# Performance work log

Hardware: AMD Instinct MI355X
Metric: run time of the kernel (lower is better)

Reference implementation:

```python
import jax, jax.numpy as jnp
import numpy as np

B, S, OBS, H, A, L = 512, 512, 64, 128, 9, 2
LN_EPS = 1e-5


def setup_inputs() -> dict:
    key = jax.random.key(0)
    ks = jax.random.split(key, 32)
    sc = 0.05
    inp = {
        'obs': jax.random.normal(ks[0], (B, S, OBS), jnp.float32),
        'masks': (jax.random.uniform(ks[1], (B, S)) > 0.01).astype(jnp.float32),
        'noise': jax.random.normal(ks[2], (B, S, A), jnp.float32),
        # encoder: Linear(OBS,H) -> LayerNorm(H) -> ReLU -> Linear(H,H) -> ReLU
        'enc_w1': jax.random.normal(ks[3], (H, OBS)) * sc,
        'enc_b1': jnp.zeros((H,)),
        'ln_g': jnp.ones((H,)),
        'ln_b': jnp.zeros((H,)),
        'enc_w2': jax.random.normal(ks[4], (H, H)) * sc,
        'enc_b2': jnp.zeros((H,)),
        # 2-layer LSTM, torch gate order [i, f, g, o]
        'wih0': jax.random.normal(ks[5], (4 * H, H)) * sc,
        'whh0': jax.random.normal(ks[6], (4 * H, H)) * sc,
        'bih0': jnp.zeros((4 * H,)),
        'bhh0': jnp.zeros((4 * H,)),
        'wih1': jax.random.normal(ks[7], (4 * H, H)) * sc,
        'whh1': jax.random.normal(ks[8], (4 * H, H)) * sc,
        'bih1': jnp.zeros((4 * H,)),
        'bhh1': jnp.zeros((4 * H,)),
        # actor mean head: Linear(H,H//2) -> ReLU -> Linear(H//2,A) -> Tanh
        'am_w1': jax.random.normal(ks[9], (H // 2, H)) * sc,
        'am_b1': jnp.zeros((H // 2,)),
        'am_w2': jax.random.normal(ks[10], (A, H // 2)) * sc,
        'am_b2': jnp.zeros((A,)),
        'log_std': jnp.full((A,), -1.0, jnp.float32),
        # critic head: Linear(H,H//2) -> ReLU -> Linear(H//2,1)
        'cr_w1': jax.random.normal(ks[11], (H // 2, H)) * sc,
        'cr_b1': jnp.zeros((H // 2,)),
        'cr_w2': jax.random.normal(ks[12], (1, H // 2)) * sc,
        'cr_b2': jnp.zeros((1,)),
    }
    return inp


def _encoder(x, w1, b1, g, b, w2, b2):
    y = x @ w1.T + b1
    mu = y.mean(-1, keepdims=True)
    var = y.var(-1, keepdims=True)
    y = (y - mu) * jax.lax.rsqrt(var + LN_EPS) * g + b
    y = jax.nn.relu(y)
    return jax.nn.relu(y @ w2.T + b2)


def _masked_lstm(enc, masks, wih, whh, bih, bhh):
    # enc: (B,S,H), masks: (B,S). Carry h,c: (L,B,H). Reset h,c by mask, then step.
    h0 = jnp.zeros((L, enc.shape[0], H), enc.dtype)
    c0 = jnp.zeros_like(h0)

    def step(carry, xs):
        h, c = carry
        x_t, m_t = xs  # (B,H), (B,1)
        h = h * m_t
        c = c * m_t
        hs, cs = [], []
        inp = x_t
        for l in range(L):
            gates = inp @ wih[l].T + bih[l] + h[l] @ whh[l].T + bhh[l]
            i, f, g, o = jnp.split(gates, 4, axis=-1)
            c_l = jax.nn.sigmoid(f) * c[l] + jax.nn.sigmoid(i) * jnp.tanh(g)
            h_l = jax.nn.sigmoid(o) * jnp.tanh(c_l)
            hs.append(h_l)
            cs.append(c_l)
            inp = h_l
        return (jnp.stack(hs), jnp.stack(cs)), inp

    xs = (enc.transpose(1, 0, 2), masks.T[:, :, None])  # time-major
    (h, c), outs = jax.lax.scan(step, (h0, c0), xs)
    return outs.transpose(1, 0, 2), h, c  # (B,S,H)


def reference(obs, masks, noise, enc_w1, enc_b1, ln_g, ln_b, enc_w2, enc_b2,
              wih0, whh0, bih0, bhh0, wih1, whh1, bih1, bhh1,
              am_w1, am_b1, am_w2, am_b2, log_std, cr_w1, cr_b1, cr_w2, cr_b2):
    enc = _encoder(obs, enc_w1, enc_b1, ln_g, ln_b, enc_w2, enc_b2)
    lstm_out, h, c = _masked_lstm(enc, masks, (wih0, wih1), (whh0, whh1),
                                  (bih0, bih1), (bhh0, bhh1))
    mean = jnp.tanh(jax.nn.relu(lstm_out @ am_w1.T + am_b1) @ am_w2.T + am_b2)
    ls = jnp.clip(log_std, -4.0, 0.0)
    std = jnp.exp(ls)
    action = jax.lax.stop_gradient(mean + std * noise)  # dist.sample()
    z = (action - mean) / std
    log_prob = (-0.5 * z * z - ls - 0.5 * jnp.log(2.0 * jnp.pi)).sum(-1)
    value = (jax.nn.relu(lstm_out @ cr_w1.T + cr_b1) @ cr_w2.T + cr_b2)[..., 0]
    return action, log_prob, value, h, c
```

## Files before the change

kernel.cpp:

```cpp
#include <hip/hip_runtime.h>
#include <hip/hip_bf16.h>
#include <math.h>


#define DEV __device__ __forceinline__

typedef __attribute__((ext_vector_type(4))) float f4;
typedef __attribute__((ext_vector_type(8))) short s16x8;

static constexpr int Bsz = 512, Ssz = 512, OBSD = 64, HD = 128, AD = 9;
static constexpr int TOK = Bsz * Ssz;

static constexpr size_t LP_OFF  = (size_t)TOK * AD;
static constexpr size_t VAL_OFF = LP_OFF + TOK;
static constexpr size_t H_OFF   = VAL_OFF + TOK;
static constexpr size_t C_OFF   = H_OFF + 2 * Bsz * HD;

static constexpr size_t WS_SEQ   = 0;
static constexpr size_t WS_WIH1B = (size_t)TOK * HD * 2;
static constexpr size_t WS_AMW1B = WS_WIH1B + 512 * 128 * 2;
static constexpr size_t WS_AMW2P = WS_AMW1B + 64 * 128 * 2;
static constexpr size_t WS_CRW1B = WS_AMW2P + 16 * 64 * 2;
static constexpr size_t WS_CRW2P = WS_CRW1B + 64 * 128 * 2;

static constexpr int L_H0  = 131072;
static constexpr int L_H1  = 139264;
static constexpr int L_MKB = 147456;
static constexpr int L_TOT = 149504;

DEV unsigned short f2bf(float f) {
  union { float f; unsigned u; } v; v.f = f;
  unsigned r = v.u + 0x7fffu + ((v.u >> 16) & 1u);
  return (unsigned short)(r >> 16);
}
DEV s16x8 cvt8(f4 a, f4 b) {
  s16x8 r;
  r[0]=(short)f2bf(a[0]); r[1]=(short)f2bf(a[1]); r[2]=(short)f2bf(a[2]); r[3]=(short)f2bf(a[3]);
  r[4]=(short)f2bf(b[0]); r[5]=(short)f2bf(b[1]); r[6]=(short)f2bf(b[2]); r[7]=(short)f2bf(b[3]);
  return r;
}
DEV f4 splat4(float v) { f4 r = {v, v, v, v}; return r; }
DEV f4 mfma16(s16x8 a, s16x8 b, f4 c) {
  return __builtin_amdgcn_mfma_f32_16x16x32_bf16(a, b, c, 0, 0, 0);
}
DEV float fexp2(float x) { return __builtin_amdgcn_exp2f(x); }
DEV float frcp(float x)  { return __builtin_amdgcn_rcpf(x); }
DEV float sigm(float x)   { return frcp(1.f + fexp2(-1.4426950408889634f * x)); }
DEV float tanh_f(float x) { return 2.f * frcp(1.f + fexp2(-2.8853900817779268f * x)) - 1.f; }

__global__ void k_prep(const float* __restrict__ wih1, const float* __restrict__ amw1,
                       const float* __restrict__ amw2, const float* __restrict__ crw1,
                       const float* __restrict__ crw2,
                       unsigned short* __restrict__ wih1b, unsigned short* __restrict__ amw1b,
                       unsigned short* __restrict__ amw2p, unsigned short* __restrict__ crw1b,
                       unsigned short* __restrict__ crw2p)
{
  int i = blockIdx.x * 256 + threadIdx.x;
  if (i < 65536) wih1b[i] = f2bf(wih1[i]);
  if (i < 8192) { amw1b[i] = f2bf(amw1[i]); crw1b[i] = f2bf(crw1[i]); }
  if (i < 1024) {
    int n = i >> 6, k = i & 63;
    amw2p[i] = (n < 9) ? f2bf(amw2[n * 64 + k]) : (unsigned short)0;
    crw2p[i] = (n == 0) ? f2bf(crw2[k]) : (unsigned short)0;
  }
}

__global__ __launch_bounds__(256) void k_encoder(
    const float* __restrict__ obs,
    const float* __restrict__ w1, const float* __restrict__ b1,
    const float* __restrict__ lng, const float* __restrict__ lnb,
    const float* __restrict__ w2, const float* __restrict__ b2,
    unsigned short* __restrict__ enc)
{
  __shared__ unsigned short sy[4][2048];
  const int tid = threadIdx.x, lane = tid & 63, wv = tid >> 6;
  const int cl = lane & 15, grp = lane >> 4;
  const size_t tok0 = ((size_t)blockIdx.x * 4 + wv) * 16;

  s16x8 aob[2];
  {
    const float* p = obs + (tok0 + cl) * 64 + grp * 8;
    aob[0] = cvt8(*(const f4*)p, *(const f4*)(p + 4));
    aob[1] = cvt8(*(const f4*)(p + 32), *(const f4*)(p + 36));
  }

  f4 acc[8];
#pragma unroll
  for (int n = 0; n < 8; ++n) acc[n] = splat4(0.f);
#pragma unroll
  for (int kk = 0; kk < 2; ++kk)
#pragma unroll
    for (int n = 0; n < 8; ++n) {
      const float* p = w1 + (size_t)(n * 16 + cl) * 64 + kk * 32 + grp * 8;
      acc[n] = mfma16(aob[kk], cvt8(*(const f4*)p, *(const f4*)(p + 4)), acc[n]);
    }

  float y[8][4], s[4] = {0,0,0,0}, q[4] = {0,0,0,0};
#pragma unroll
  for (int n = 0; n < 8; ++n) {
    float bb = b1[n * 16 + cl];
#pragma unroll
    for (int i = 0; i < 4; ++i) { float v = acc[n][i] + bb; y[n][i] = v; s[i] += v; q[i] += v * v; }
  }
#pragma unroll
  for (int i = 0; i < 4; ++i)
    for (int m = 1; m < 16; m <<= 1) { s[i] += __shfl_xor(s[i], m); q[i] += __shfl_xor(q[i], m); }
  float mean[4], rstd[4];
#pragma unroll
  for (int i = 0; i < 4; ++i) {
    mean[i] = s[i] * (1.f / 128.f);
    float var = q[i] * (1.f / 128.f) - mean[i] * mean[i];
    rstd[i] = rsqrtf(var + 1e-5f);
  }
  unsigned short* my = sy[wv];
#pragma unroll
  for (int n = 0; n < 8; ++n) {
    float gg = lng[n * 16 + cl], bb = lnb[n * 16 + cl];
#pragma unroll
    for (int i = 0; i < 4; ++i) {
      float v = (y[n][i] - mean[i]) * rstd[i] * gg + bb;
      v = v > 0.f ? v : 0.f;
      int row = grp * 4 + i;
      *(unsigned short*)((char*)my + row * 256 + (((n * 16 + cl) * 2) ^ ((row & 7) << 4))) = f2bf(v);
    }
  }
  __syncthreads();

  f4 acc2[8];
#pragma unroll
  for (int n = 0; n < 8; ++n) acc2[n] = splat4(0.f);
#pragma unroll
  for (int kk = 0; kk < 4; ++kk) {
    s16x8 a2 = *(const s16x8*)((char*)my + cl * 256 + ((kk * 64 + grp * 16) ^ ((cl & 7) << 4)));
#pragma unroll
    for (int n = 0; n < 8; ++n) {
      const float* p = w2 + (size_t)(n * 16 + cl) * 128 + kk * 32 + grp * 8;
      acc2[n] = mfma16(a2, cvt8(*(const f4*)p, *(const f4*)(p + 4)), acc2[n]);
    }
  }
#pragma unroll
  for (int n = 0; n < 8; ++n) {
    float bb = b2[n * 16 + cl];
#pragma unroll
    for (int i = 0; i < 4; ++i) {
      float v = acc2[n][i] + bb; v = v > 0.f ? v : 0.f;
      enc[(tok0 + grp * 4 + i) * 128 + n * 16 + cl] = f2bf(v);
    }
  }
}

__global__ __launch_bounds__(512, 2) void k_lstm(
    const unsigned short* enc_in,
    unsigned short* lstm_out,
    const float* __restrict__ masks,
    const float* __restrict__ wih0f, const float* __restrict__ whh0f,
    const float* __restrict__ bih0, const float* __restrict__ bhh0,
    const unsigned short* __restrict__ wih1b, const float* __restrict__ whh1f,
    const float* __restrict__ bih1, const float* __restrict__ bhh1,
    float* __restrict__ out_h, float* __restrict__ out_c)
{
  extern __shared__ char sm[];
  unsigned int* s_mkb = (unsigned int*)(sm + L_MKB);

  const int tid = threadIdx.x, lane = tid & 63, wv = tid >> 6;
  const int cl = lane & 15, grp = lane >> 4;
  const int b0 = blockIdx.x * 16, u0 = wv * 16;
  const s16x8 z8 = {0,0,0,0,0,0,0,0};

  for (int idx = tid; idx < 8192; idx += 512) {
    int row = idx >> 4, c8 = idx & 15;
    const float* p = wih0f + (size_t)row * 128 + c8 * 8;
    s16x8 v = cvt8(*(const f4*)p, *(const f4*)(p + 4));
    *(s16x8*)(sm + row * 256 + ((c8 * 16) ^ ((row & 7) << 4))) = v;
  }
  for (int idx = tid; idx < 4096; idx += 512)
    ((unsigned int*)(sm + L_H0))[idx] = 0;
  {
    int t = tid;
    unsigned int m = 0;
#pragma unroll
    for (int r = 0; r < 16; ++r)
      m |= (masks[(size_t)(b0 + r) * 512 + t] != 0.f ? 1u : 0u) << r;
    s_mkb[t] = m;
  }

  s16x8 Bh0[4][4], Bh1[4][4];
#pragma unroll
  for (int g = 0; g < 4; ++g)
#pragma unroll
    for (int kk = 0; kk < 4; ++kk) {
      const float* p0 = whh0f + (size_t)(g * 128 + u0 + cl) * 128 + kk * 32 + grp * 8;
      Bh0[g][kk] = cvt8(*(const f4*)p0, *(const f4*)(p0 + 4));
      const float* p1 = whh1f + (size_t)(g * 128 + u0 + cl) * 128 + kk * 32 + grp * 8;
      Bh1[g][kk] = cvt8(*(const f4*)p1, *(const f4*)(p1 + 4));
    }
  float bias0[4], bias1[4];
#pragma unroll
  for (int g = 0; g < 4; ++g) {
    bias0[g] = bih0[g * 128 + u0 + cl] + bhh0[g * 128 + u0 + cl];
    bias1[g] = bih1[g * 128 + u0 + cl] + bhh1[g * 128 + u0 + cl];
  }
  float c0[4] = {0,0,0,0}, c1[4] = {0,0,0,0};
  float h0r[4] = {0,0,0,0}, h1r[4] = {0,0,0,0};

  const int swz = (cl & 7) << 4;
  int hoff[4];
#pragma unroll
  for (int kk = 0; kk < 4; ++kk) hoff[kk] = cl * 256 + ((kk * 64 + grp * 16) ^ swz);
  const char* w0l = sm + (u0 + cl) * 256;
  const unsigned short* encl = enc_in + (size_t)(b0 + cl) * 65536 + grp * 8;
  const unsigned short* w1l = wih1b + (size_t)(u0 + cl) * 128 + grp * 8;

  const int srow = tid >> 5, sj = tid & 31;
  const int sdso = srow * 256 + ((sj * 8) ^ ((srow & 7) << 4));
  unsigned short* souts = lstm_out + (size_t)(b0 + srow) * 65536 + sj * 4;

  __syncthreads();

  s16x8 axc[4];
#pragma unroll
  for (int kk = 0; kk < 4; ++kk) axc[kk] = *(const s16x8*)(encl + kk * 32);

  for (int t = 0; t < 512; ++t) {
    const int par = t & 1;
    char* h0p = sm + L_H0 + (par ^ 1) * 4096;
    char* h0c = sm + L_H0 + par * 4096;
    char* h1p = sm + L_H1 + (par ^ 1) * 4096;
    char* h1c = sm + L_H1 + par * 4096;

    if (t > 0) {
      unsigned long long v = *(const unsigned long long*)(h1p + sdso);
      *(unsigned long long*)(souts + (size_t)(t - 1) * 128) = v;
    }

    s16x8 axn[4];
    {
      const unsigned short* pe = encl + (size_t)(t + (t < 511 ? 1 : 0)) * 128;
#pragma unroll
      for (int kk = 0; kk < 4; ++kk) axn[kk] = *(const s16x8*)(pe + kk * 32);
    }

    const unsigned int mk = s_mkb[t];
    const int mA = (mk >> cl) & 1;
    float mc[4];
#pragma unroll
    for (int i = 0; i < 4; ++i) mc[i] = (mk >> (grp * 4 + i)) & 1 ? 1.f : 0.f;

    f4 acc[4];
#pragma unroll
    for (int g = 0; g < 4; ++g) acc[g] = splat4(bias0[g]);
    s16x8 ah[4];
#pragma unroll
    for (int kk = 0; kk < 4; ++kk) {
      ah[kk] = *(const s16x8*)(h0p + hoff[kk]);
      if (!mA) ah[kk] = z8;
    }
#pragma unroll
    for (int kk = 0; kk < 4; ++kk)
#pragma unroll
      for (int g = 0; g < 4; ++g) {
        s16x8 bw = *(const s16x8*)(w0l + g * 32768 + ((kk * 64 + grp * 16) ^ swz));
        acc[g] = mfma16(axc[kk], bw, acc[g]);
        acc[g] = mfma16(ah[kk], Bh0[g][kk], acc[g]);
      }

    s16x8 bx1[4][4];
#pragma unroll
    for (int g = 0; g < 4; ++g)
#pragma unroll
      for (int kk = 0; kk < 4; ++kk)
        bx1[g][kk] = *(const s16x8*)(w1l + g * 16384 + kk * 32);

#pragma unroll
    for (int i = 0; i < 4; ++i) {
      float ig = sigm(acc[0][i]), fg = sigm(acc[1][i]);
      float gg = tanh_f(acc[2][i]), og = sigm(acc[3][i]);
      float c = fg * (c0[i] * mc[i]) + ig * gg;
      c0[i] = c; h0r[i] = og * tanh_f(c);
    }
#pragma unroll
    for (int i = 0; i < 4; ++i) {
      int row = grp * 4 + i;
      *(unsigned short*)(h0c + row * 256 + (((u0 + cl) * 2) ^ ((row & 7) << 4))) = f2bf(h0r[i]);
    }
    __syncthreads();

#pragma unroll
    for (int g = 0; g < 4; ++g) acc[g] = splat4(bias1[g]);
    s16x8 ax1[4], ah1[4];
#pragma unroll
    for (int kk = 0; kk < 4; ++kk) {
      ax1[kk] = *(const s16x8*)(h0c + hoff[kk]);
      ah1[kk] = *(const s16x8*)(h1p + hoff[kk]);
      if (!mA) ah1[kk] = z8;
    }
#pragma unroll
    for (int g = 0; g < 4; ++g)
#pragma unroll
      for (int kk = 0; kk < 4; ++kk) {
        acc[g] = mfma16(ax1[kk], bx1[g][kk], acc[g]);
        acc[g] = mfma16(ah1[kk], Bh1[g][kk], acc[g]);
      }
#pragma unroll
    for (int i = 0; i < 4; ++i) {
      float ig = sigm(acc[0][i]), fg = sigm(acc[1][i]);
      float gg = tanh_f(acc[2][i]), og = sigm(acc[3][i]);
      float c = fg * (c1[i] * mc[i]) + ig * gg;
      c1[i] = c; h1r[i] = og * tanh_f(c);
    }
#pragma unroll
    for (int i = 0; i < 4; ++i) {
      int row = grp * 4 + i;
      *(unsigned short*)(h1c + row * 256 + (((u0 + cl) * 2) ^ ((row & 7) << 4))) = f2bf(h1r[i]);
    }
#pragma unroll
    for (int kk = 0; kk < 4; ++kk) axc[kk] = axn[kk];
    __syncthreads();
  }

  {
    unsigned long long v = *(const unsigned long long*)(sm + L_H1 + 4096 + sdso);
    *(unsigned long long*)(souts + (size_t)511 * 128) = v;
  }

#pragma unroll
  for (int i = 0; i < 4; ++i) {
    size_t b = (size_t)b0 + grp * 4 + i;
    out_h[b * 128 + u0 + cl]         = h0r[i];
    out_h[65536 + b * 128 + u0 + cl] = h1r[i];
    out_c[b * 128 + u0 + cl]         = c0[i];
    out_c[65536 + b * 128 + u0 + cl] = c1[i];
  }
}

__global__ __launch_bounds__(256) void k_heads(
    const unsigned short* __restrict__ lo,
    const float* __restrict__ noise,
    const unsigned short* __restrict__ amw1b, const float* __restrict__ am_b1,
    const unsigned short* __restrict__ amw2p, const float* __restrict__ am_b2,
    const float* __restrict__ log_std,
    const unsigned short* __restrict__ crw1b, const float* __restrict__ cr_b1,
    const unsigned short* __restrict__ crw2p, const float* __restrict__ cr_b2,
    float* __restrict__ out)
{
  __shared__ unsigned short sha[4][1024];
  __shared__ unsigned short shc[4][1024];
  const int tid = threadIdx.x, lane = tid & 63, wv = tid >> 6;
  const int cl = lane & 15, grp = lane >> 4;
  const size_t tok0 = ((size_t)blockIdx.x * 4 + wv) * 16;

  s16x8 a[4];
  {
    const unsigned short* p = lo + (tok0 + cl) * 128 + grp * 8;
#pragma unroll
    for (int kk = 0; kk < 4; ++kk) a[kk] = *(const s16x8*)(p + kk * 32);
  }

  f4 acc[4], accc[4];
#pragma unroll
  for (int n = 0; n < 4; ++n) { acc[n] = splat4(0.f); accc[n] = splat4(0.f); }
#pragma unroll
  for (int kk = 0; kk < 4; ++kk)
#pragma unroll
    for (int n = 0; n < 4; ++n) {
      acc[n]  = mfma16(a[kk], *(const s16x8*)(amw1b + (size_t)(n * 16 + cl) * 128 + kk * 32 + grp * 8), acc[n]);
      accc[n] = mfma16(a[kk], *(const s16x8*)(crw1b + (size_t)(n * 16 + cl) * 128 + kk * 32 + grp * 8), accc[n]);
    }
#pragma unroll
  for (int n = 0; n < 4; ++n) {
    float ba = am_b1[n * 16 + cl], bc = cr_b1[n * 16 + cl];
#pragma unroll
    for (int i = 0; i < 4; ++i) {
      int row = grp * 4 + i;
      int off = row * 128 + (((n * 16 + cl) * 2) ^ ((row & 7) << 4));
      float va = acc[n][i] + ba;  va = va > 0.f ? va : 0.f;
      float vc = accc[n][i] + bc; vc = vc > 0.f ? vc : 0.f;
      *(unsigned short*)((char*)sha[wv] + off) = f2bf(va);
      *(unsigned short*)((char*)shc[wv] + off) = f2bf(vc);
    }
  }
  __syncthreads();

  f4 am = splat4(0.f), vv = splat4(0.f);
#pragma unroll
  for (int kk = 0; kk < 2; ++kk) {
    int off = cl * 128 + ((kk * 64 + grp * 16) ^ ((cl & 7) << 4));
    s16x8 a2 = *(const s16x8*)((char*)sha[wv] + off);
    s16x8 c2 = *(const s16x8*)((char*)shc[wv] + off);
    am = mfma16(a2, *(const s16x8*)(amw2p + (size_t)cl * 64 + kk * 32 + grp * 8), am);
    vv = mfma16(c2, *(const s16x8*)(crw2p + (size_t)cl * 64 + kk * 32 + grp * 8), vv);
  }

  float ls = 0.f, stdv = 0.f, b2a = 0.f;
  if (cl < 9) {
    float l = log_std[cl];
    ls = fminf(fmaxf(l, -4.f), 0.f);
    stdv = fexp2(ls * 1.4426950408889634f);
    b2a = am_b2[cl];
  }
  float crb2 = cr_b2[0];
#pragma unroll
  for (int i = 0; i < 4; ++i) {
    size_t tok = tok0 + grp * 4 + i;
    float lp = 0.f;
    if (cl < 9) {
      float meanv = tanh_f(am[i] + b2a);
      float nz = noise[tok * 9 + cl];
      float act = meanv + stdv * nz;
      float z = (act - meanv) / stdv;
      lp = -0.5f * z * z - ls - 0.91893853320467274f;
      out[tok * 9 + cl] = act;
    }
#pragma unroll
    for (int m = 1; m < 16; m <<= 1) lp += __shfl_xor(lp, m);
    if (cl == 0) {
      out[LP_OFF + tok]  = lp;
      out[VAL_OFF + tok] = vv[i] + crb2;
    }
  }
}

extern "C" void kernel_launch(void* const* d_in, const int* in_sizes, int n_in,
                              void* d_out, int out_size, void* d_ws, size_t ws_size,
                              hipStream_t stream)
{
  const float* obs     = (const float*)d_in[0];
  const float* masks   = (const float*)d_in[1];
  const float* noise   = (const float*)d_in[2];
  const float* enc_w1  = (const float*)d_in[3];
  const float* enc_b1  = (const float*)d_in[4];
  const float* ln_g    = (const float*)d_in[5];
  const float* ln_b    = (const float*)d_in[6];
  const float* enc_w2  = (const float*)d_in[7];
  const float* enc_b2  = (const float*)d_in[8];
  const float* wih0    = (const float*)d_in[9];
  const float* whh0    = (const float*)d_in[10];
  const float* bih0    = (const float*)d_in[11];
  const float* bhh0    = (const float*)d_in[12];
  const float* wih1    = (const float*)d_in[13];
  const float* whh1    = (const float*)d_in[14];
  const float* bih1    = (const float*)d_in[15];
  const float* bhh1    = (const float*)d_in[16];
  const float* am_w1   = (const float*)d_in[17];
  const float* am_b1   = (const float*)d_in[18];
  const float* am_w2   = (const float*)d_in[19];
  const float* am_b2   = (const float*)d_in[20];
  const float* log_std = (const float*)d_in[21];
  const float* cr_w1   = (const float*)d_in[22];
  const float* cr_b1   = (const float*)d_in[23];
  const float* cr_w2   = (const float*)d_in[24];
  const float* cr_b2   = (const float*)d_in[25];

  char* ws = (char*)d_ws;
  unsigned short* seq   = (unsigned short*)(ws + WS_SEQ);
  unsigned short* wih1b = (unsigned short*)(ws + WS_WIH1B);
  unsigned short* amw1b = (unsigned short*)(ws + WS_AMW1B);
  unsigned short* amw2p = (unsigned short*)(ws + WS_AMW2P);
  unsigned short* crw1b = (unsigned short*)(ws + WS_CRW1B);
  unsigned short* crw2p = (unsigned short*)(ws + WS_CRW2P);
  float* out            = (float*)d_out;

  hipFuncSetAttribute((const void*)k_lstm, hipFuncAttributeMaxDynamicSharedMemorySize, L_TOT);

  k_prep<<<256, 256, 0, stream>>>(wih1, am_w1, am_w2, cr_w1, cr_w2,
                                  wih1b, amw1b, amw2p, crw1b, crw2p);
  k_encoder<<<4096, 256, 0, stream>>>(obs, enc_w1, enc_b1, ln_g, ln_b, enc_w2, enc_b2, seq);
  k_lstm<<<32, 512, L_TOT, stream>>>(seq, seq, masks, wih0, whh0, bih0, bhh0,
                                     wih1b, whh1, bih1, bhh1, out + H_OFF, out + C_OFF);
  k_heads<<<4096, 256, 0, stream>>>(seq, noise, amw1b, am_b1, amw2p, am_b2, log_std,
                                    crw1b, cr_b1, crw2p, cr_b2, out);
}
```

Before: 2.659 ms.

## Precompute next-step layer-0 input projection inside layer-1 phase of LSTM loop

The layer-0 input-projection MFMAs (enc x Wih0) for step t+1 are now computed during layer 1 of step t and carried in a separate accumulator, taking them off the serial h-dependent critical path of layer 0. The layer-1 input weights are loaded in two halves to lower register pressure, and the encoder prefetch distance grows to two steps. In exchange the kernel keeps more live accumulator registers and adds a prologue, which may hurt occupancy or cause spills.

```diff
diff --git a/kernel.cpp b/kernel.cpp
--- a/kernel.cpp
+++ b/kernel.cpp
@@ -217,9 +217,24 @@
 
   __syncthreads();
 
-  s16x8 axc[4];
-#pragma unroll
-  for (int kk = 0; kk < 4; ++kk) axc[kk] = *(const s16x8*)(encl + kk * 32);
+  f4 xacc[4];
+#pragma unroll
+  for (int g = 0; g < 4; ++g) xacc[g] = splat4(bias0[g]);
+  {
+    s16x8 ax0[4];
+#pragma unroll
+    for (int kk = 0; kk < 4; ++kk) ax0[kk] = *(const s16x8*)(encl + kk * 32);
+#pragma unroll
+    for (int kk = 0; kk < 4; ++kk)
+#pragma unroll
+      for (int g = 0; g < 4; ++g) {
+        s16x8 bw = *(const s16x8*)(w0l + g * 32768 + ((kk * 64 + grp * 16) ^ swz));
+        xacc[g] = mfma16(ax0[kk], bw, xacc[g]);
+      }
+  }
+  s16x8 axn[4];
+#pragma unroll
+  for (int kk = 0; kk < 4; ++kk) axn[kk] = *(const s16x8*)(encl + 128 + kk * 32);
 
   for (int t = 0; t < 512; ++t) {
     const int par = t & 1;
@@ -233,13 +248,6 @@
       *(unsigned long long*)(souts + (size_t)(t - 1) * 128) = v;
     }
 
-    s16x8 axn[4];
-    {
-      const unsigned short* pe = encl + (size_t)(t + (t < 511 ? 1 : 0)) * 128;
-#pragma unroll
-      for (int kk = 0; kk < 4; ++kk) axn[kk] = *(const s16x8*)(pe + kk * 32);
-    }
-
     const unsigned int mk = s_mkb[t];
     const int mA = (mk >> cl) & 1;
     float mc[4];
@@ -248,7 +256,9 @@
 
     f4 acc[4];
 #pragma unroll
-    for (int g = 0; g < 4; ++g) acc[g] = splat4(bias0[g]);
+    for (int g = 0; g < 4; ++g) acc[g] = xacc[g];
+#pragma unroll
+    for (int g = 0; g < 4; ++g) xacc[g] = splat4(bias0[g]);
     s16x8 ah[4];
 #pragma unroll
     for (int kk = 0; kk < 4; ++kk) {
@@ -258,18 +268,15 @@
 #pragma unroll
     for (int kk = 0; kk < 4; ++kk)
 #pragma unroll
-      for (int g = 0; g < 4; ++g) {
-        s16x8 bw = *(const s16x8*)(w0l + g * 32768 + ((kk * 64 + grp * 16) ^ swz));
-        acc[g] = mfma16(axc[kk], bw, acc[g]);
+      for (int g = 0; g < 4; ++g)
         acc[g] = mfma16(ah[kk], Bh0[g][kk], acc[g]);
-      }
-
-    s16x8 bx1[4][4];
-#pragma unroll
-    for (int g = 0; g < 4; ++g)
+
+    s16x8 bx1[2][4];
+#pragma unroll
+    for (int g2 = 0; g2 < 2; ++g2)
 #pragma unroll
       for (int kk = 0; kk < 4; ++kk)
-        bx1[g][kk] = *(const s16x8*)(w1l + g * 16384 + kk * 32);
+        bx1[g2][kk] = *(const s16x8*)(w1l + g2 * 16384 + kk * 32);
 
 #pragma unroll
     for (int i = 0; i < 4; ++i) {
@@ -295,11 +302,36 @@
       if (!mA) ah1[kk] = z8;
     }
 #pragma unroll
-    for (int g = 0; g < 4; ++g)
-#pragma unroll
-      for (int kk = 0; kk < 4; ++kk) {
-        acc[g] = mfma16(ax1[kk], bx1[g][kk], acc[g]);
-        acc[g] = mfma16(ah1[kk], Bh1[g][kk], acc[g]);
+    for (int kk = 0; kk < 4; ++kk)
+#pragma unroll
+      for (int g2 = 0; g2 < 2; ++g2) {
+        acc[g2] = mfma16(ax1[kk], bx1[g2][kk], acc[g2]);
+        acc[g2] = mfma16(ah1[kk], Bh1[g2][kk], acc[g2]);
+      }
+#pragma unroll
+    for (int g2 = 0; g2 < 2; ++g2)
+#pragma unroll
+      for (int kk = 0; kk < 4; ++kk)
+        bx1[g2][kk] = *(const s16x8*)(w1l + (2 + g2) * 16384 + kk * 32);
+#pragma unroll
+    for (int kk = 0; kk < 4; ++kk)
+#pragma unroll
+      for (int g = 0; g < 4; ++g) {
+        s16x8 bw = *(const s16x8*)(w0l + g * 32768 + ((kk * 64 + grp * 16) ^ swz));
+        xacc[g] = mfma16(axn[kk], bw, xacc[g]);
+      }
+    {
+      const int tn = (t + 2 < 512) ? t + 2 : 511;
+      const unsigned short* pe = encl + (size_t)tn * 128;
+#pragma unroll
+      for (int kk = 0; kk < 4; ++kk) axn[kk] = *(const s16x8*)(pe + kk * 32);
+    }
+#pragma unroll
+    for (int kk = 0; kk < 4; ++kk)
+#pragma unroll
+      for (int g2 = 0; g2 < 2; ++g2) {
+        acc[2 + g2] = mfma16(ax1[kk], bx1[g2][kk], acc[2 + g2]);
+        acc[2 + g2] = mfma16(ah1[kk], Bh1[2 + g2][kk], acc[2 + g2]);
       }
 #pragma unroll
     for (int i = 0; i < 4; ++i) {
@@ -313,8 +345,6 @@
       int row = grp * 4 + i;
       *(unsigned short*)(h1c + row * 256 + (((u0 + cl) * 2) ^ ((row & 7) << 4))) = f2bf(h1r[i]);
     }
-#pragma unroll
-    for (int kk = 0; kk < 4; ++kk) axc[kk] = axn[kk];
     __syncthreads();
   }
 
```

New measurement: 3.169 ms. +19.2%, slower.
